# Performance work log

Measured on AMD Instinct MI355X. Metric: run time of the kernel, lower is better.

Reference implementation:

```python
import jax, jax.numpy as jnp
import numpy as np

N = 100000
E = 640000
IN_CH = 256
OUT_CH = 64
HID = 2 * OUT_CH  # 128


def setup_inputs() -> dict:
    key = jax.random.key(0)
    ks = jax.random.split(key, 8)
    x = jax.random.normal(ks[0], (N, IN_CH), dtype=jnp.float32)
    edge_index = jax.random.randint(ks[1], (2, E), 0, N, dtype=jnp.int32)
    s = 1.0 / np.sqrt(IN_CH)
    W1 = jax.random.uniform(ks[2], (IN_CH, HID), jnp.float32, -s, s)
    b1 = jnp.zeros((HID,), jnp.float32)
    s2 = 1.0 / np.sqrt(HID)
    W_mu = jax.random.uniform(ks[3], (HID, OUT_CH), jnp.float32, -s2, s2)
    b_mu = jnp.zeros((OUT_CH,), jnp.float32)
    W_ls = jax.random.uniform(ks[4], (HID, OUT_CH), jnp.float32, -s2, s2)
    b_ls = jnp.zeros((OUT_CH,), jnp.float32)
    return {"x": x, "W1": W1, "b1": b1, "W_mu": W_mu, "b_mu": b_mu,
            "W_ls": W_ls, "b_ls": b_ls, "edge_index": edge_index}


def _gcn_norm(edge_index, n_nodes):
    # PyG GCNConv default: add self-loops, symmetric normalization D^-1/2 A D^-1/2
    loops = jnp.arange(n_nodes, dtype=edge_index.dtype)
    src = jnp.concatenate([edge_index[0], loops])
    dst = jnp.concatenate([edge_index[1], loops])
    deg = jax.ops.segment_sum(jnp.ones_like(dst, jnp.float32), dst, num_segments=n_nodes)
    dinv = jnp.where(deg > 0, jax.lax.rsqrt(deg), 0.0)
    norm = dinv[src] * dinv[dst]  # [E+N]
    return src, dst, norm


def _gcn_conv(x, W, b, src, dst, norm, n_nodes):
    h = x @ W                                   # [N, F_out]
    msg = h[src] * norm[:, None]                # [E+N, F_out] gather
    out = jax.ops.segment_sum(msg, dst, num_segments=n_nodes)  # scatter-add
    return out + b


def reference(x, W1, b1, W_mu, b_mu, W_ls, b_ls, edge_index):
    src, dst, norm = _gcn_norm(edge_index, N)
    h = jax.nn.relu(_gcn_conv(x, W1, b1, src, dst, norm, N))
    mu = _gcn_conv(h, W_mu, b_mu, src, dst, norm, N)
    logstd = _gcn_conv(h, W_ls, b_ls, src, dst, norm, N)
    return mu, logstd
```

## Files before the change

### kernel.cpp

```cpp
#include <hip/hip_runtime.h>
#include <math.h>

#define NN 100000
#define EE 640000
#define INCH 256
#define HIDC 128
#define OUTC 64
#define NCHUNK ((NN + 255) / 256)

typedef __attribute__((ext_vector_type(8))) short short8;
typedef __attribute__((ext_vector_type(8))) unsigned short ushort8;
typedef __attribute__((ext_vector_type(4))) float floatx4;

__device__ __forceinline__ short f2bf(float f) {
    unsigned u = __float_as_uint(f);
    u += 0x7fff + ((u >> 16) & 1);
    return (short)(u >> 16);
}

__device__ __forceinline__ float bf2f(unsigned short u) {
    return __uint_as_float(((unsigned)u) << 16);
}

__device__ __forceinline__ unsigned pk2bf(float lo, float hi) {
    unsigned r;
    asm("v_cvt_pk_bf16_f32 %0, %1, %2" : "=v"(r) : "v"(lo), "v"(hi));
    return r;
}

__device__ __forceinline__ void async_copy16(const void* g, void* l) {
    __builtin_amdgcn_global_load_lds(
        (const __attribute__((address_space(1))) unsigned int*)g,
        (__attribute__((address_space(3))) unsigned int*)l,
        16, 0, 0);
}

__global__ void k_deg_count(const int* __restrict__ dstp, int* __restrict__ deg) {
    int e = blockIdx.x * 256 + threadIdx.x;
    if (e < EE) atomicAdd(&deg[dstp[e]], 1);
}

__global__ __launch_bounds__(256) void k_scan1(const int* __restrict__ deg,
                                               int* __restrict__ partials,
                                               const float* __restrict__ W1,
                                               const float* __restrict__ Wmu,
                                               const float* __restrict__ bmu,
                                               const float* __restrict__ Wls,
                                               const float* __restrict__ bls,
                                               short* __restrict__ wt,
                                               short* __restrict__ wct,
                                               float* __restrict__ bcat) {
    int i = blockIdx.x * 256 + threadIdx.x;
    if (i < 32768) {
        int n = i >> 8, k = i & 255;
        wt[i] = f2bf(W1[k * HIDC + n]);
    } else if (i < 49152) {
        int j = i - 32768;
        int n = j >> 7, k = j & 127;
        float v = (n < OUTC) ? Wmu[k * OUTC + n] : Wls[k * OUTC + (n - OUTC)];
        wct[j] = f2bf(v);
    } else if (i < 49280) {
        int c = i - 49152;
        bcat[c] = (c < OUTC) ? bmu[c] : bls[c - OUTC];
    }
    int v = (i < NN) ? deg[i] : 0;
    for (int o = 32; o; o >>= 1) v += __shfl_down(v, o, 64);
    __shared__ int sm[4];
    if ((threadIdx.x & 63) == 0) sm[threadIdx.x >> 6] = v;
    __syncthreads();
    if (threadIdx.x == 0) partials[blockIdx.x] = sm[0] + sm[1] + sm[2] + sm[3];
}

__global__ __launch_bounds__(256) void k_scan3(const int* __restrict__ deg,
                                               const int* __restrict__ partials,
                                               int* __restrict__ row_off,
                                               int* __restrict__ cursor,
                                               float* __restrict__ dinv) {
    int t = threadIdx.x;
    int pacc = 0;
    for (int b = t; b < blockIdx.x; b += 256) pacc += partials[b];
    for (int o = 32; o; o >>= 1) pacc += __shfl_down(pacc, o, 64);
    __shared__ int pg[4];
    if ((t & 63) == 0) pg[t >> 6] = pacc;
    __syncthreads();
    int blockoff = pg[0] + pg[1] + pg[2] + pg[3];
    int i = blockIdx.x * 256 + t;
    int v = (i < NN) ? deg[i] : 0;
    __shared__ int sm[256];
    sm[t] = v;
    __syncthreads();
    for (int o = 1; o < 256; o <<= 1) {
        int add = (t >= o) ? sm[t - o] : 0;
        __syncthreads();
        sm[t] += add;
        __syncthreads();
    }
    if (i < NN) {
        int excl = blockoff + sm[t] - v;
        row_off[i] = excl;
        cursor[i] = excl;
        dinv[i] = rsqrtf((float)(v + 1));
    }
}

__global__ void k_fill(const int* __restrict__ srcp, const int* __restrict__ dstp,
                       int* __restrict__ cursor, int* __restrict__ esrc) {
    int e = blockIdx.x * 256 + threadIdx.x;
    if (e < EE) {
        int d = dstp[e];
        int pos = atomicAdd(&cursor[d], 1);
        esrc[pos] = srcp[e];
    }
}

__global__ __launch_bounds__(256, 4) void k_mgemm1(const float* __restrict__ x,
                                                   const short* __restrict__ wt,
                                                   short* __restrict__ out) {
    __shared__ __align__(16) float xs[2][32 * 128];
    int wave = threadIdx.x >> 6;
    int lane = threadIdx.x & 63;
    int m = lane & 15, quad = lane >> 4;
    int rbase = blockIdx.x * 32;

#pragma unroll
    for (int i = 0; i < 4; i++) {
        int r = wave * 8 + 2 * i + (lane >> 5);
        int chunk = (lane & 31) ^ (r & 7);
        const float* gsrc = x + (size_t)(rbase + r) * INCH + chunk * 4;
        float* ldst = xs[0] + (wave * 8 + 2 * i) * 128;
        async_copy16(gsrc, ldst);
    }

    short8 bfr[2][8];
#pragma unroll
    for (int ct = 0; ct < 2; ct++)
#pragma unroll
        for (int kg = 0; kg < 8; kg++)
            bfr[ct][kg] = *(const short8*)(wt + (size_t)(wave * 32 + ct * 16 + m) * INCH
                                              + kg * 32 + quad * 8);

#pragma unroll
    for (int i = 0; i < 4; i++) {
        int r = wave * 8 + 2 * i + (lane >> 5);
        int chunk = (lane & 31) ^ (r & 7);
        const float* gsrc = x + (size_t)(rbase + r) * INCH + 128 + chunk * 4;
        float* ldst = xs[1] + (wave * 8 + 2 * i) * 128;
        async_copy16(gsrc, ldst);
    }

    floatx4 acc[2][2];
#pragma unroll
    for (int rt = 0; rt < 2; rt++) { acc[rt][0] = (floatx4)(0.f); acc[rt][1] = (floatx4)(0.f); }

#define COMPUTE_HALF(h)                                                                  \
    _Pragma("unroll")                                                                    \
    for (int k0 = 0; k0 < 4; k0++) {                                                     \
        int cb = k0 * 8 + (quad << 1);                       \
        _Pragma("unroll")                                                                \
        for (int rt = 0; rt < 2; rt++) {                                                 \
            int r = rt * 16 + m;                                                         \
            int key = m & 7;                                                             \
            const float* p0 = xs[h] + r * 128 + (((cb) ^ key) << 2);                     \
            const float* p1 = xs[h] + r * 128 + (((cb + 1) ^ key) << 2);                 \
            float4 f0 = *(const float4*)p0;                                              \
            float4 f1 = *(const float4*)p1;                                              \
            union { short8 s; unsigned u[4]; } a;                                        \
            a.u[0] = pk2bf(f0.x, f0.y); a.u[1] = pk2bf(f0.z, f0.w);                      \
            a.u[2] = pk2bf(f1.x, f1.y); a.u[3] = pk2bf(f1.z, f1.w);                      \
            acc[rt][0] = __builtin_amdgcn_mfma_f32_16x16x32_bf16(a.s, bfr[0][(h)*4+k0],  \
                                                                 acc[rt][0], 0, 0, 0);   \
            acc[rt][1] = __builtin_amdgcn_mfma_f32_16x16x32_bf16(a.s, bfr[1][(h)*4+k0],  \
                                                                 acc[rt][1], 0, 0, 0);   \
        }                                                                                \
    }

    asm volatile("s_waitcnt vmcnt(4)" ::: "memory");
    __builtin_amdgcn_sched_barrier(0);
    __builtin_amdgcn_s_barrier();
    COMPUTE_HALF(0)
    asm volatile("s_waitcnt vmcnt(0)" ::: "memory");
    __builtin_amdgcn_sched_barrier(0);
    __builtin_amdgcn_s_barrier();
    COMPUTE_HALF(1)
#undef COMPUTE_HALF

#pragma unroll
    for (int rt = 0; rt < 2; rt++) {
        int rs = rbase + rt * 16 + quad * 4;
#pragma unroll
        for (int ct = 0; ct < 2; ct++) {
            int c = wave * 32 + ct * 16 + m;
#pragma unroll
            for (int r = 0; r < 4; r++) {
                out[(size_t)(rs + r) * HIDC + c] = f2bf(acc[rt][ct][r]);
            }
        }
    }
}

__global__ __launch_bounds__(256, 1) void k_mgemm2(const short* __restrict__ agg,
                                                   const short* __restrict__ wct,
                                                   const float* __restrict__ bcat,
                                                   float* __restrict__ out) {
    int wave = threadIdx.x >> 6;
    int lane = threadIdx.x & 63;
    int rhalf = wave & 1, chalf = wave >> 1;
    int m = lane & 15, quad = lane >> 4;
    int rbase = blockIdx.x * 64 + rhalf * 32;
    int r0c = min(rbase + m, NN - 1);
    int r1c = min(rbase + 16 + m, NN - 1);
    const short* ar0 = agg + (size_t)r0c * HIDC + quad * 8;
    const short* ar1 = agg + (size_t)r1c * HIDC + quad * 8;

    short8 pa0[4], pa1[4];
#pragma unroll
    for (int c = 0; c < 4; c++) {
        pa0[c] = *(const short8*)(ar0 + c * 32);
        pa1[c] = *(const short8*)(ar1 + c * 32);
    }
    __builtin_amdgcn_sched_barrier(0);

    const short* wbase = wct + quad * 8 + (size_t)m * HIDC + (size_t)(chalf * 4) * 16 * HIDC;
    floatx4 acc0[4], acc1[4];
#pragma unroll
    for (int i = 0; i < 4; i++) { acc0[i] = (floatx4)(0.f); acc1[i] = (floatx4)(0.f); }
#pragma unroll
    for (int k = 0; k < 4; k++) {
        const short* wq = wbase + k * 32;
#pragma unroll
        for (int nt = 0; nt < 4; nt++) {
            short8 b = *(const short8*)(wq + (size_t)nt * 16 * HIDC);
            acc0[nt] = __builtin_amdgcn_mfma_f32_16x16x32_bf16(pa0[k], b, acc0[nt], 0, 0, 0);
            acc1[nt] = __builtin_amdgcn_mfma_f32_16x16x32_bf16(pa1[k], b, acc1[nt], 0, 0, 0);
        }
    }
    int rs0 = rbase + quad * 4;
    int rs1 = rbase + 16 + quad * 4;
#pragma unroll
    for (int nt = 0; nt < 4; nt++) {
        int c = (chalf * 4 + nt) * 16 + m;
        float bv = bcat[c];
        float* obase = (c < OUTC) ? (out + c) : (out + (size_t)NN * OUTC + (c - OUTC));
#pragma unroll
        for (int r = 0; r < 4; r++) {
            int rr = rs0 + r;
            if (rr < NN) obase[(size_t)rr * OUTC] = acc0[nt][r] + bv;
            int rr2 = rs1 + r;
            if (rr2 < NN) obase[(size_t)rr2 * OUTC] = acc1[nt][r] + bv;
        }
    }
}

template <bool RELU>
__global__ __launch_bounds__(256) void k_gather(const short* __restrict__ feat,
                                                const int* __restrict__ esrc,
                                                const int* __restrict__ row_off,
                                                const int* __restrict__ deg,
                                                const float* __restrict__ dinv,
                                                const float* __restrict__ bias,
                                                short* __restrict__ out) {
    int gid = blockIdx.x * 256 + threadIdx.x;
    int d = gid >> 4;
    int l = threadIdx.x & 15;
    if (d >= NN) return;
    const ushort8* fp = (const ushort8*)feat;
    float dd = dinv[d];
    float sw = dd * dd;
    ushort8 sv = fp[(size_t)d * 16 + l];
    float acc[8];
#pragma unroll
    for (int i = 0; i < 8; i++) acc[i] = bf2f(sv[i]) * sw;
    int off = row_off[d];
    int cnt = deg[d];
    for (int base = 0; base < cnt; base += 16) {
        int mm = min(16, cnt - base);
        int sj = (l < mm) ? esrc[off + base + l] : 0;
        float dj = (l < mm) ? dinv[sj] : 0.f;
        int j = 0;
        for (; j + 4 <= mm; j += 4) {
            int s0 = __shfl(sj, j + 0, 16);
            int s1 = __shfl(sj, j + 1, 16);
            int s2 = __shfl(sj, j + 2, 16);
            int s3 = __shfl(sj, j + 3, 16);
            float n0 = __shfl(dj, j + 0, 16) * dd;
            float n1 = __shfl(dj, j + 1, 16) * dd;
            float n2 = __shfl(dj, j + 2, 16) * dd;
            float n3 = __shfl(dj, j + 3, 16) * dd;
            ushort8 v0 = fp[(size_t)s0 * 16 + l];
            ushort8 v1 = fp[(size_t)s1 * 16 + l];
            ushort8 v2 = fp[(size_t)s2 * 16 + l];
            ushort8 v3 = fp[(size_t)s3 * 16 + l];
#pragma unroll
            for (int i = 0; i < 8; i++) acc[i] = fmaf(bf2f(v0[i]), n0, acc[i]);
#pragma unroll
            for (int i = 0; i < 8; i++) acc[i] = fmaf(bf2f(v1[i]), n1, acc[i]);
#pragma unroll
            for (int i = 0; i < 8; i++) acc[i] = fmaf(bf2f(v2[i]), n2, acc[i]);
#pragma unroll
            for (int i = 0; i < 8; i++) acc[i] = fmaf(bf2f(v3[i]), n3, acc[i]);
        }
        if (j + 2 <= mm) {
            int s0 = __shfl(sj, j + 0, 16);
            int s1 = __shfl(sj, j + 1, 16);
            float n0 = __shfl(dj, j + 0, 16) * dd;
            float n1 = __shfl(dj, j + 1, 16) * dd;
            ushort8 v0 = fp[(size_t)s0 * 16 + l];
            ushort8 v1 = fp[(size_t)s1 * 16 + l];
#pragma unroll
            for (int i = 0; i < 8; i++) acc[i] = fmaf(bf2f(v0[i]), n0, acc[i]);
#pragma unroll
            for (int i = 0; i < 8; i++) acc[i] = fmaf(bf2f(v1[i]), n1, acc[i]);
            j += 2;
        }
        if (j < mm) {
            int s0 = __shfl(sj, j, 16);
            float n0 = __shfl(dj, j, 16) * dd;
            ushort8 v0 = fp[(size_t)s0 * 16 + l];
#pragma unroll
            for (int i = 0; i < 8; i++) acc[i] = fmaf(bf2f(v0[i]), n0, acc[i]);
        }
    }
    if (RELU) {
        float4 b0 = *(const float4*)(bias + l * 8);
        float4 b1 = *(const float4*)(bias + l * 8 + 4);
        acc[0] = fmaxf(acc[0] + b0.x, 0.f);
        acc[1] = fmaxf(acc[1] + b0.y, 0.f);
        acc[2] = fmaxf(acc[2] + b0.z, 0.f);
        acc[3] = fmaxf(acc[3] + b0.w, 0.f);
        acc[4] = fmaxf(acc[4] + b1.x, 0.f);
        acc[5] = fmaxf(acc[5] + b1.y, 0.f);
        acc[6] = fmaxf(acc[6] + b1.z, 0.f);
        acc[7] = fmaxf(acc[7] + b1.w, 0.f);
    }
    ushort8 o;
#pragma unroll
    for (int i = 0; i < 8; i++) o[i] = (unsigned short)f2bf(acc[i]);
    ((ushort8*)out)[(size_t)d * 16 + l] = o;
}

extern "C" void kernel_launch(void* const* d_in, const int* in_sizes, int n_in,
                              void* d_out, int out_size, void* d_ws, size_t ws_size,
                              hipStream_t stream) {
    const float* x   = (const float*)d_in[0];
    const float* W1  = (const float*)d_in[1];
    const float* b1  = (const float*)d_in[2];
    const float* Wmu = (const float*)d_in[3];
    const float* bmu = (const float*)d_in[4];
    const float* Wls = (const float*)d_in[5];
    const float* bls = (const float*)d_in[6];
    const int*   ei  = (const int*)d_in[7];
    const int* srcp = ei;
    const int* dstp = ei + EE;

    float* out = (float*)d_out;

    char* wsb = (char*)d_ws;
    short* bufA    = (short*)wsb;
    short* bufH    = bufA + (size_t)NN * HIDC;
    int*   deg     = (int*)(bufH + (size_t)NN * HIDC);
    int*   row_off = deg + NN;
    int*   cursor  = row_off + NN;
    float* dinv    = (float*)(cursor + NN);
    int*   esrc    = (int*)(dinv + NN);
    int*   partials = esrc + EE;
    short* wt      = (short*)(partials + NCHUNK + 1);
    short* wct     = wt + 128 * 256;
    float* bcat    = (float*)(wct + 128 * 128);

    const int nb_e = (EE + 255) / 256;
    const int nb_g = (NN * 16) / 256;
    const int nb_m1 = NN / 32;
    const int nb_m2 = (NN + 63) / 64;

    hipMemsetAsync(deg, 0, NN * sizeof(int), stream);
    k_deg_count<<<nb_e, 256, 0, stream>>>(dstp, deg);
    k_scan1<<<NCHUNK, 256, 0, stream>>>(deg, partials, W1, Wmu, bmu, Wls, bls, wt, wct, bcat);
    k_scan3<<<NCHUNK, 256, 0, stream>>>(deg, partials, row_off, cursor, dinv);
    k_fill<<<nb_e, 256, 0, stream>>>(srcp, dstp, cursor, esrc);

    k_mgemm1<<<nb_m1, 256, 0, stream>>>(x, wt, bufA);
    k_gather<true><<<nb_g, 256, 0, stream>>>(bufA, esrc, row_off, deg, dinv, b1, bufH);

    k_gather<false><<<nb_g, 256, 0, stream>>>(bufH, esrc, row_off, deg, dinv, nullptr, bufA);
    k_mgemm2<<<nb_m2, 256, 0, stream>>>(bufA, wct, bcat, out);
}
```

Measured before the change: 348.6 us.

## Sort destination nodes by degree bucket to balance gather work

Builds a degree histogram (capped at 63) during the scan pass, computes per-bucket offsets, and uses them in the fill kernel to produce a permutation of nodes grouped by degree. Both gather kernels then process nodes in this permuted order, so the 16-lane groups that share a wavefront handle similar edge counts and diverge less. The cost is extra atomics, one tiny kernel launch, one more indirection per node, and writes to output rows that are no longer contiguous across neighbouring groups.

Result: slower. 363.3 us (+4.2%).

```diff
diff --git a/kernel.cpp b/kernel.cpp
--- a/kernel.cpp
+++ b/kernel.cpp
@@ -42,6 +42,7 @@
 
 __global__ __launch_bounds__(256) void k_scan1(const int* __restrict__ deg,
                                                int* __restrict__ partials,
+                                               int* __restrict__ hist,
                                                const float* __restrict__ W1,
                                                const float* __restrict__ Wmu,
                                                const float* __restrict__ bmu,
@@ -50,7 +51,10 @@
                                                short* __restrict__ wt,
                                                short* __restrict__ wct,
                                                float* __restrict__ bcat) {
-    int i = blockIdx.x * 256 + threadIdx.x;
+    int t = threadIdx.x;
+    int i = blockIdx.x * 256 + t;
+    __shared__ int lh[64];
+    if (t < 64) lh[t] = 0;
     if (i < 32768) {
         int n = i >> 8, k = i & 255;
         wt[i] = f2bf(W1[k * HIDC + n]);
@@ -64,11 +68,26 @@
         bcat[c] = (c < OUTC) ? bmu[c] : bls[c - OUTC];
     }
     int v = (i < NN) ? deg[i] : 0;
-    for (int o = 32; o; o >>= 1) v += __shfl_down(v, o, 64);
+    __syncthreads();
+    if (i < NN) atomicAdd(&lh[min(v, 63)], 1);
+    int s = v;
+    for (int o = 32; o; o >>= 1) s += __shfl_down(s, o, 64);
     __shared__ int sm[4];
-    if ((threadIdx.x & 63) == 0) sm[threadIdx.x >> 6] = v;
+    if ((t & 63) == 0) sm[t >> 6] = s;
     __syncthreads();
-    if (threadIdx.x == 0) partials[blockIdx.x] = sm[0] + sm[1] + sm[2] + sm[3];
+    if (t == 0) partials[blockIdx.x] = sm[0] + sm[1] + sm[2] + sm[3];
+    if (t < 64 && lh[t]) atomicAdd(&hist[t], lh[t]);
+}
+
+__global__ void k_binoff(const int* __restrict__ hist, int* __restrict__ bcur) {
+    int t = threadIdx.x;
+    int v = hist[t];
+    int s = 0;
+    for (int b = 0; b < 64; b++) {
+        int hv = __shfl(v, b, 64);
+        if (b < t) s += hv;
+    }
+    bcur[t] = s;
 }
 
 __global__ __launch_bounds__(256) void k_scan3(const int* __restrict__ deg,
@@ -103,13 +122,34 @@
     }
 }
 
-__global__ void k_fill(const int* __restrict__ srcp, const int* __restrict__ dstp,
-                       int* __restrict__ cursor, int* __restrict__ esrc) {
-    int e = blockIdx.x * 256 + threadIdx.x;
+__global__ __launch_bounds__(256) void k_fill(const int* __restrict__ srcp,
+                                              const int* __restrict__ dstp,
+                                              int* __restrict__ cursor,
+                                              int* __restrict__ esrc,
+                                              const int* __restrict__ deg,
+                                              int* __restrict__ bcur,
+                                              int* __restrict__ perm) {
+    int t = threadIdx.x;
+    int e = blockIdx.x * 256 + t;
     if (e < EE) {
         int d = dstp[e];
         int pos = atomicAdd(&cursor[d], 1);
         esrc[pos] = srcp[e];
+    }
+    __shared__ int lh[64], lbase[64];
+    bool node = ((unsigned)blockIdx.x * 256u) < NN;
+    if (node) {
+        if (t < 64) lh[t] = 0;
+        __syncthreads();
+        int my = -1, dg = 0;
+        if (e < NN) {
+            dg = min(deg[e], 63);
+            my = atomicAdd(&lh[dg], 1);
+        }
+        __syncthreads();
+        if (t < 64 && lh[t] > 0) lbase[t] = atomicAdd(&bcur[t], lh[t]);
+        __syncthreads();
+        if (e < NN) perm[lbase[dg] + my] = e;
     }
 }
 
@@ -155,7 +195,7 @@
 #define COMPUTE_HALF(h)                                                                  \
     _Pragma("unroll")                                                                    \
     for (int k0 = 0; k0 < 4; k0++) {                                                     \
-        int cb = k0 * 8 + (quad << 1);                       \
+        int cb = k0 * 8 + (quad << 1);                                                   \
         _Pragma("unroll")                                                                \
         for (int rt = 0; rt < 2; rt++) {                                                 \
             int r = rt * 16 + m;                                                         \
@@ -257,12 +297,14 @@
                                                 const int* __restrict__ row_off,
                                                 const int* __restrict__ deg,
                                                 const float* __restrict__ dinv,
+                                                const int* __restrict__ perm,
                                                 const float* __restrict__ bias,
                                                 short* __restrict__ out) {
     int gid = blockIdx.x * 256 + threadIdx.x;
-    int d = gid >> 4;
+    int ds = gid >> 4;
     int l = threadIdx.x & 15;
-    if (d >= NN) return;
+    if (ds >= NN) return;
+    int d = perm[ds];
     const ushort8* fp = (const ushort8*)feat;
     float dd = dinv[d];
     float sw = dd * dd;
@@ -366,6 +408,9 @@
     short* wt      = (short*)(partials + NCHUNK + 1);
     short* wct     = wt + 128 * 256;
     float* bcat    = (float*)(wct + 128 * 128);
+    int*   hist    = (int*)(bcat + 128);
+    int*   bcur    = hist + 64;
+    int*   perm    = bcur + 64;
 
     const int nb_e = (EE + 255) / 256;
     const int nb_g = (NN * 16) / 256;
@@ -373,14 +418,16 @@
     const int nb_m2 = (NN + 63) / 64;
 
     hipMemsetAsync(deg, 0, NN * sizeof(int), stream);
+    hipMemsetAsync(hist, 0, 64 * sizeof(int), stream);
     k_deg_count<<<nb_e, 256, 0, stream>>>(dstp, deg);
-    k_scan1<<<NCHUNK, 256, 0, stream>>>(deg, partials, W1, Wmu, bmu, Wls, bls, wt, wct, bcat);
+    k_scan1<<<NCHUNK, 256, 0, stream>>>(deg, partials, hist, W1, Wmu, bmu, Wls, bls, wt, wct, bcat);
+    k_binoff<<<1, 64, 0, stream>>>(hist, bcur);
     k_scan3<<<NCHUNK, 256, 0, stream>>>(deg, partials, row_off, cursor, dinv);
-    k_fill<<<nb_e, 256, 0, stream>>>(srcp, dstp, cursor, esrc);
+    k_fill<<<nb_e, 256, 0, stream>>>(srcp, dstp, cursor, esrc, deg, bcur, perm);
 
     k_mgemm1<<<nb_m1, 256, 0, stream>>>(x, wt, bufA);
-    k_gather<true><<<nb_g, 256, 0, stream>>>(bufA, esrc, row_off, deg, dinv, b1, bufH);
-
-    k_gather<false><<<nb_g, 256, 0, stream>>>(bufH, esrc, row_off, deg, dinv, nullptr, bufA);
+    k_gather<true><<<nb_g, 256, 0, stream>>>(bufA, esrc, row_off, deg, dinv, perm, b1, bufH);
+
+    k_gather<false><<<nb_g, 256, 0, stream>>>(bufH, esrc, row_off, deg, dinv, perm, nullptr, bufA);
     k_mgemm2<<<nb_m2, 256, 0, stream>>>(bufA, wct, bcat, out);
 }
```
